# Kernel optimization log

Hardware: AMD Instinct MI355X
Metric: run time of the kernel (lower is better)

The kernel has to match this reference:

```python
import jax, jax.numpy as jnp
import numpy as np

EMBED = 1024
HEADS = 16

def setup_inputs() -> dict:
    key = jax.random.key(0)
    ks = jax.random.split(key, 6)
    N, S = 1, 4096
    half = EMBED // 2
    x = jax.random.normal(ks[0], (N, S, EMBED), dtype=jnp.float32)
    Wq = jax.random.normal(ks[1], (half, half), dtype=jnp.float32) * 0.02
    Wk = jax.random.normal(ks[2], (half, half), dtype=jnp.float32) * 0.02
    Wv = jax.random.normal(ks[3], (half, half), dtype=jnp.float32) * 0.02
    Wo = jax.random.normal(ks[4], (EMBED, half), dtype=jnp.float32) * 0.02
    bo = jnp.zeros((EMBED,), dtype=jnp.float32)
    return {"x": x, "Wq": Wq, "Wk": Wk, "Wv": Wv, "Wo": Wo, "bo": bo}

def reference(x, Wq, Wk, Wv, Wo, bo):
    N, S, E = x.shape
    H = HEADS
    Dh = (E // 2) // H                 # per-head dim of the half-width projections (32)
    scale = float(E // H) ** 0.5       # original scales by head_dim = embed/heads = 64
    left = x[..., : E // 2]            # only the left chunk feeds attention in the source
    # torch Linear: y = x @ W.T (no bias)
    q = (left @ Wq.T).reshape(N, S, H, Dh)
    k = (left @ Wk.T).reshape(N, S, H, Dh)
    v = (left @ Wv.T).reshape(N, S, H, Dh)
    energy = jnp.einsum('nqhd,nkhd->nqkh', q, k)          # [N,S,S,H] full score tensor
    att = jax.nn.softmax(energy / scale, axis=2)          # softmax over key axis
    out = jnp.einsum('nqkh,nkhd->nqhd', att, v)           # [N,S,H,Dh]
    out = out.reshape(N, S, E // 2)
    return out @ Wo.T + bo                                # fc_out: half -> embed
```

## Files before the change

### kernel.cpp

```cpp
#include <hip/hip_runtime.h>
#include <stdint.h>


#define SEQ    4096
#define DMODEL 1024
#define DHALF  512
#define NH     16
#define DH     32

typedef __attribute__((ext_vector_type(4))) float facc4;
typedef __attribute__((ext_vector_type(8))) short bfrag8;

#define MFMA_BF16(a, b, c) __builtin_amdgcn_mfma_f32_16x16x32_bf16((a), (b), (c), 0, 0, 0)

static __device__ __forceinline__ uint16_t f2b(float x) {
    uint32_t u = __float_as_uint(x);
    return (uint16_t)((u + 0x7FFFu + ((u >> 16) & 1u)) >> 16);
}
static __device__ __forceinline__ float b2f(uint16_t b) {
    return __uint_as_float(((uint32_t)b) << 16);
}

static __device__ __forceinline__ bfrag8 cvt8perm(float4 a, float4 b) {
    uint32_t u0 = __float_as_uint(a.x) + 0x8000u, u1 = __float_as_uint(a.y) + 0x8000u;
    uint32_t u2 = __float_as_uint(a.z) + 0x8000u, u3 = __float_as_uint(a.w) + 0x8000u;
    uint32_t u4 = __float_as_uint(b.x) + 0x8000u, u5 = __float_as_uint(b.y) + 0x8000u;
    uint32_t u6 = __float_as_uint(b.z) + 0x8000u, u7 = __float_as_uint(b.w) + 0x8000u;
    union { uint32_t w[4]; bfrag8 r; } u;
    u.w[0] = __builtin_amdgcn_perm(u1, u0, 0x07060302u);
    u.w[1] = __builtin_amdgcn_perm(u3, u2, 0x07060302u);
    u.w[2] = __builtin_amdgcn_perm(u5, u4, 0x07060302u);
    u.w[3] = __builtin_amdgcn_perm(u7, u6, 0x07060302u);
    return u.r;
}

__global__ __launch_bounds__(256) void convert_w(
    const float* __restrict__ Wq, const float* __restrict__ Wk,
    const float* __restrict__ Wv, const float* __restrict__ Wo,
    const float* __restrict__ x,
    uint16_t* __restrict__ q, uint16_t* __restrict__ k,
    uint16_t* __restrict__ v, uint16_t* __restrict__ o,
    uint16_t* __restrict__ xb)
{
    int zz = blockIdx.x;
    if (zz >= 640) {
        size_t g = (size_t)(zz - 640) * 2048 + (size_t)threadIdx.x * 8;
        int row = (int)(g >> 9);
        int col = (int)(g & 511);
        const float* src = &x[(size_t)row * DMODEL + col];
        float4 a = *(const float4*)src;
        float4 b = *(const float4*)(src + 4);
        *(bfrag8*)&xb[g] = cvt8perm(a, b);
        return;
    }
    const float* src; uint16_t* dst; size_t off;
    if      (zz < 128) { src = Wq; dst = q; off = (size_t)zz * 2048; }
    else if (zz < 256) { src = Wk; dst = k; off = (size_t)(zz - 128) * 2048; }
    else if (zz < 384) { src = Wv; dst = v; off = (size_t)(zz - 256) * 2048; }
    else               { src = Wo; dst = o; off = (size_t)(zz - 384) * 2048; }
    size_t i = off + (size_t)threadIdx.x * 8;
    float4 a = *(const float4*)&src[i];
    float4 b = *(const float4*)&src[i + 4];
    *(bfrag8*)&dst[i] = cvt8perm(a, b);
}

__device__ __forceinline__ void gemm128(
    const uint16_t* __restrict__ A, int lda,
    const uint16_t* __restrict__ B, int ldb,
    void* __restrict__ C, int ldc, int cF32,
    const float* __restrict__ bias, float scale,
    int Kd, int m0, int n0)
{
    __shared__ __align__(16) uint16_t As[2][128 * 40];
    __shared__ __align__(16) uint16_t Bs[2][128 * 40];

    const int tid  = threadIdx.x;
    const int lane = tid & 63;
    const int wv   = tid >> 6;
    const int lo   = lane & 15;
    const int quad = lane >> 4;
    const int srow = tid >> 2;
    const int skq  = (tid & 3) * 8;
    const int rb   = (wv >> 1) * 64;
    const int cb   = (wv & 1) * 64;

    const facc4 ZACC = {0.f, 0.f, 0.f, 0.f};
    facc4 acc[4][4];
#pragma unroll
    for (int i = 0; i < 4; ++i)
#pragma unroll
        for (int j = 0; j < 4; ++j) acc[i][j] = ZACC;

    const uint16_t* hA0 = &A[(size_t)(m0 + srow) * lda + skq];
    const uint16_t* hA1 = &A[(size_t)(m0 + srow + 64) * lda + skq];
    const uint16_t* pB0 = &B[(size_t)(n0 + srow) * ldb + skq];
    const uint16_t* pB1 = &B[(size_t)(n0 + srow + 64) * ldb + skq];

    bfrag8 ra0 = *(const bfrag8*)hA0;
    bfrag8 ra1 = *(const bfrag8*)hA1;
    bfrag8 rb0 = *(const bfrag8*)pB0;
    bfrag8 rb1 = *(const bfrag8*)pB1;

    *(bfrag8*)&As[0][srow * 40 + skq]        = ra0;
    *(bfrag8*)&As[0][(srow + 64) * 40 + skq] = ra1;
    *(bfrag8*)&Bs[0][srow * 40 + skq]        = rb0;
    *(bfrag8*)&Bs[0][(srow + 64) * 40 + skq] = rb1;
    __syncthreads();

    int p = 0;
    for (int kt = 0; kt < Kd; kt += 32) {
        const bool more = (kt + 32 < Kd);
        if (more) {
            ra0 = *(const bfrag8*)(hA0 + kt + 32);
            ra1 = *(const bfrag8*)(hA1 + kt + 32);
            rb0 = *(const bfrag8*)(pB0 + kt + 32);
            rb1 = *(const bfrag8*)(pB1 + kt + 32);
        }

        bfrag8 af[4], bf[4];
#pragma unroll
        for (int i = 0; i < 4; ++i) {
            af[i] = *(const bfrag8*)&As[p][(rb + i * 16 + lo) * 40 + quad * 8];
            bf[i] = *(const bfrag8*)&Bs[p][(cb + i * 16 + lo) * 40 + quad * 8];
        }
#pragma unroll
        for (int i = 0; i < 4; ++i)
#pragma unroll
            for (int j = 0; j < 4; ++j)
                acc[i][j] = MFMA_BF16(af[i], bf[j], acc[i][j]);

        if (more) {
            *(bfrag8*)&As[1 - p][srow * 40 + skq]        = ra0;
            *(bfrag8*)&As[1 - p][(srow + 64) * 40 + skq] = ra1;
            *(bfrag8*)&Bs[1 - p][srow * 40 + skq]        = rb0;
            *(bfrag8*)&Bs[1 - p][(srow + 64) * 40 + skq] = rb1;
            __syncthreads();
            p ^= 1;
        }
    }

#pragma unroll
    for (int j = 0; j < 4; ++j) {
        int col  = n0 + cb + j * 16 + lo;
        float bv = bias ? bias[col] : 0.f;
#pragma unroll
        for (int i = 0; i < 4; ++i) {
#pragma unroll
            for (int r = 0; r < 4; ++r) {
                int row = m0 + rb + i * 16 + quad * 4 + r;
                float v = acc[i][j][r] * scale + bv;
                if (cF32) ((float*)C)[(size_t)row * ldc + col] = v;
                else      ((uint16_t*)C)[(size_t)row * ldc + col] = f2b(v);
            }
        }
    }
}

#define SC_Q (0.125f * 1.4426950408889634f)

__global__ __launch_bounds__(256, 2) void qkv_kernel(
    const uint16_t* __restrict__ xb,
    const uint16_t* __restrict__ Wqb, const uint16_t* __restrict__ Wkb,
    const uint16_t* __restrict__ Wvb,
    uint16_t* __restrict__ Q, uint16_t* __restrict__ K, uint16_t* __restrict__ V)
{
    const int z = blockIdx.z;
    const uint16_t* W = (z == 0) ? Wqb : (z == 1) ? Wkb : Wvb;
    uint16_t* Out     = (z == 0) ? Q   : (z == 1) ? K   : V;
    float scale       = (z == 0) ? SC_Q : 1.0f;
    gemm128(xb, DHALF, W, DHALF, Out, DHALF, 0, nullptr, scale, DHALF,
            blockIdx.y * 128, blockIdx.x * 128);
}

__global__ __launch_bounds__(256, 2) void outproj_kernel(
    const uint16_t* __restrict__ O, const uint16_t* __restrict__ Wob,
    const float* __restrict__ bo, float* __restrict__ Y)
{
    gemm128(O, DHALF, Wob, DHALF, Y, DMODEL, 1, bo, 1.0f, DHALF,
            blockIdx.y * 128, blockIdx.x * 128);
}

__global__ __launch_bounds__(256) void attn_kernel(
    const uint16_t* __restrict__ Q, const uint16_t* __restrict__ Kb,
    const uint16_t* __restrict__ Vb, uint16_t* __restrict__ Op,
    float* __restrict__ lbuf, int kspan)
{
    __shared__ __align__(16) uint16_t Ks[2][64 * 40];
    __shared__ __align__(16) uint16_t Vt[2][32 * 64];

    const int tid  = threadIdx.x;
    const int lane = tid & 63;
    const int wv   = tid >> 6;
    const int lo   = lane & 15;
    const int quad = lane >> 4;

    const int f  = blockIdx.x + 32 * blockIdx.y + 512 * blockIdx.z;
    const int pp = (f & 7) | ((f >> 8) << 3);
    const int h  = pp & 15;
    const int sp = pp >> 4;
    const int q0 = ((f >> 3) & 31) * 128;

    const int srow = tid >> 2;
    const int skq  = (tid & 3) * 8;

    const facc4 ZACC = {0.f, 0.f, 0.f, 0.f};

    bfrag8 qf[2];
    qf[0] = *(const bfrag8*)&Q[(size_t)(q0 + wv * 32 + lo) * DHALF + h * DH + quad * 8];
    qf[1] = *(const bfrag8*)&Q[(size_t)(q0 + wv * 32 + 16 + lo) * DHALF + h * DH + quad * 8];

    bfrag8 ones;
#pragma unroll
    for (int j = 0; j < 8; ++j) ones[j] = (short)0x3F80;

    int vt_w[8];
    {
        int pb = ((srow >> 5) << 2) | ((srow >> 2) & 3);
        int pw = (((srow >> 4) & 1) << 2) | (srow & 3);
#pragma unroll
        for (int j = 0; j < 8; ++j) {
            int d  = skq + j;
            int Rd = ((d & 7) + 2 * (d >> 3)) & 7;
            vt_w[j] = d * 64 + (((pb + Rd) & 7) << 3) + pw;
        }
    }
    int vt_r[2][2];
#pragma unroll
    for (int dt = 0; dt < 2; ++dt) {
        int d  = dt * 16 + lo;
        int Rd = ((d & 7) + 2 * (d >> 3)) & 7;
#pragma unroll
        for (int c = 0; c < 2; ++c)
            vt_r[c][dt] = d * 64 + ((((c * 4 + quad) + Rd) & 7) << 3);
    }
    const int ks_r = lo * 40 + quad * 8;

    const uint16_t* kp = &Kb[(size_t)(sp * kspan + srow) * DHALF + h * DH + skq];
    const uint16_t* vp = &Vb[(size_t)(sp * kspan + srow) * DHALF + h * DH + skq];

    facc4 oacc[2][2], oaccL[2];
    oacc[0][0] = ZACC; oacc[0][1] = ZACC;
    oacc[1][0] = ZACC; oacc[1][1] = ZACC;
    oaccL[0] = ZACC; oaccL[1] = ZACC;

    float4 kreg = *(const float4*)kp;
    float4 vreg = *(const float4*)vp;
    kp += 64 * DHALF;
    vp += 64 * DHALF;

#define STAGE(BUF) do {                                                       \
        *(float4*)&Ks[BUF][srow * 40 + skq] = kreg;                           \
        const uint16_t* vsp = (const uint16_t*)&vreg;                         \
        _Pragma("unroll")                                                     \
        for (int j = 0; j < 8; ++j) Vt[BUF][vt_w[j]] = vsp[j];                \
    } while (0)

#define TILE(BUF) do {                                                        \
        uint2 w0[4], w1[4];                                                   \
        _Pragma("unroll")                                                     \
        for (int t4 = 0; t4 < 4; ++t4) {                                      \
            bfrag8 kf = *(const bfrag8*)&Ks[BUF][t4 * 640 + ks_r];            \
            facc4 s0 = MFMA_BF16(kf, qf[0], ZACC);                            \
            facc4 s1 = MFMA_BF16(kf, qf[1], ZACC);                            \
            uint32_t a0 = __float_as_uint(__builtin_amdgcn_exp2f(s0[0])) + 0x8000u; \
            uint32_t a1 = __float_as_uint(__builtin_amdgcn_exp2f(s0[1])) + 0x8000u; \
            uint32_t a2 = __float_as_uint(__builtin_amdgcn_exp2f(s0[2])) + 0x8000u; \
            uint32_t a3 = __float_as_uint(__builtin_amdgcn_exp2f(s0[3])) + 0x8000u; \
            w0[t4].x = __builtin_amdgcn_perm(a1, a0, 0x07060302u);            \
            w0[t4].y = __builtin_amdgcn_perm(a3, a2, 0x07060302u);            \
            uint32_t b0 = __float_as_uint(__builtin_amdgcn_exp2f(s1[0])) + 0x8000u; \
            uint32_t b1 = __float_as_uint(__builtin_amdgcn_exp2f(s1[1])) + 0x8000u; \
            uint32_t b2 = __float_as_uint(__builtin_amdgcn_exp2f(s1[2])) + 0x8000u; \
            uint32_t b3 = __float_as_uint(__builtin_amdgcn_exp2f(s1[3])) + 0x8000u; \
            w1[t4].x = __builtin_amdgcn_perm(b1, b0, 0x07060302u);            \
            w1[t4].y = __builtin_amdgcn_perm(b3, b2, 0x07060302u);            \
        }                                                                     \
        union PU { uint2 u2[2]; bfrag8 f; } pu;                               \
        bfrag8 pf0[2], pf1[2];                                                \
        pu.u2[0] = w0[0]; pu.u2[1] = w0[1]; pf0[0] = pu.f;                    \
        pu.u2[0] = w0[2]; pu.u2[1] = w0[3]; pf0[1] = pu.f;                    \
        pu.u2[0] = w1[0]; pu.u2[1] = w1[1]; pf1[0] = pu.f;                    \
        pu.u2[0] = w1[2]; pu.u2[1] = w1[3]; pf1[1] = pu.f;                    \
        _Pragma("unroll")                                                     \
        for (int c = 0; c < 2; ++c) {                                         \
            _Pragma("unroll")                                                 \
            for (int dt = 0; dt < 2; ++dt) {                                  \
                bfrag8 vf = *(const bfrag8*)&Vt[BUF][vt_r[c][dt]];            \
                oacc[0][dt] = MFMA_BF16(pf0[c], vf, oacc[0][dt]);             \
                oacc[1][dt] = MFMA_BF16(pf1[c], vf, oacc[1][dt]);             \
            }                                                                 \
            oaccL[0] = MFMA_BF16(pf0[c], ones, oaccL[0]);                     \
            oaccL[1] = MFMA_BF16(pf1[c], ones, oaccL[1]);                     \
        }                                                                     \
    } while (0)

    STAGE(0);
    __syncthreads();

    const int nt = kspan >> 6;
    for (int t = 0; t < nt; t += 2) {
        kreg = *(const float4*)kp;
        vreg = *(const float4*)vp;
        kp += 64 * DHALF; vp += 64 * DHALF;
        TILE(0);
        STAGE(1);
        __syncthreads();

        const bool more = (t + 2 < nt);
        if (more) {
            kreg = *(const float4*)kp;
            vreg = *(const float4*)vp;
            kp += 64 * DHALF; vp += 64 * DHALF;
        }
        TILE(1);
        if (more) {
            STAGE(0);
            __syncthreads();
        }
    }
#undef STAGE
#undef TILE

    if (lo == 0) {
#pragma unroll
        for (int g = 0; g < 2; ++g)
#pragma unroll
            for (int r = 0; r < 4; ++r)
                lbuf[((size_t)sp * NH + h) * SEQ + q0 + wv * 32 + g * 16 + quad * 4 + r] =
                    oaccL[g][r];
    }

    uint16_t* Od = Op + (size_t)sp * SEQ * DHALF;
#pragma unroll
    for (int g = 0; g < 2; ++g) {
#pragma unroll
        for (int r = 0; r < 4; ++r) {
            int row = q0 + wv * 32 + g * 16 + quad * 4 + r;
            Od[(size_t)row * DHALF + h * DH + lo]      = f2b(oacc[g][0][r]);
            Od[(size_t)row * DHALF + h * DH + 16 + lo] = f2b(oacc[g][1][r]);
        }
    }
}

__global__ __launch_bounds__(256) void combine_kernel(
    const uint16_t* __restrict__ Op, const float* __restrict__ lbuf,
    uint16_t* __restrict__ O, int ns)
{
    int t   = blockIdx.x * 256 + threadIdx.x;
    int row = t >> 6;
    int cb  = (t & 63) << 3;
    int h   = cb >> 5;
    float l = 0.f;
    float acc[8] = {0.f, 0.f, 0.f, 0.f, 0.f, 0.f, 0.f, 0.f};
    for (int sp = 0; sp < ns; ++sp) {
        l += lbuf[((size_t)sp * NH + h) * SEQ + row];
        bfrag8 a = *(const bfrag8*)&Op[(size_t)sp * SEQ * DHALF + (size_t)row * DHALF + cb];
#pragma unroll
        for (int j = 0; j < 8; ++j) acc[j] += b2f((uint16_t)a[j]);
    }
    float inv = 1.0f / l;
    bfrag8 o;
#pragma unroll
    for (int j = 0; j < 8; ++j) o[j] = (short)f2b(acc[j] * inv);
    *(bfrag8*)&O[(size_t)row * DHALF + cb] = o;
}

extern "C" void kernel_launch(void* const* d_in, const int* in_sizes, int n_in,
                              void* d_out, int out_size, void* d_ws, size_t ws_size,
                              hipStream_t stream)
{
    const float* x  = (const float*)d_in[0];
    const float* Wq = (const float*)d_in[1];
    const float* Wk = (const float*)d_in[2];
    const float* Wv = (const float*)d_in[3];
    const float* Wo = (const float*)d_in[4];
    const float* bo = (const float*)d_in[5];

    size_t fixed_e = 3 * (size_t)DHALF * DHALF + (size_t)DMODEL * DHALF
                   + 4 * (size_t)SEQ * DHALF;
    size_t need4 = (fixed_e + 4 * (size_t)SEQ * DHALF) * 2
                 + 4 * (size_t)NH * SEQ * 4;
    const int ns = (ws_size >= need4) ? 4 : 2;

    uint16_t* Wqb = (uint16_t*)d_ws;
    uint16_t* Wkb = Wqb + (size_t)DHALF * DHALF;
    uint16_t* Wvb = Wkb + (size_t)DHALF * DHALF;
    uint16_t* Wob = Wvb + (size_t)DHALF * DHALF;
    uint16_t* Q   = Wob + (size_t)DMODEL * DHALF;
    uint16_t* K   = Q + (size_t)SEQ * DHALF;
    uint16_t* V   = K + (size_t)SEQ * DHALF;
    uint16_t* O   = V + (size_t)SEQ * DHALF;
    uint16_t* Op  = O + (size_t)SEQ * DHALF;
    float*  lbuf  = (float*)(Op + (size_t)ns * SEQ * DHALF);
    uint16_t* xb  = O;

    convert_w<<<1664, 256, 0, stream>>>(Wq, Wk, Wv, Wo, x, Wqb, Wkb, Wvb, Wob, xb);
    qkv_kernel<<<dim3(DHALF / 128, SEQ / 128, 3), 256, 0, stream>>>(
        xb, Wqb, Wkb, Wvb, Q, K, V);
    attn_kernel<<<dim3(SEQ / 128, NH, ns), 256, 0, stream>>>(Q, K, V, Op, lbuf, SEQ / ns);
    combine_kernel<<<1024, 256, 0, stream>>>(Op, lbuf, O, ns);
    outproj_kernel<<<dim3(DMODEL / 128, SEQ / 128), 256, 0, stream>>>(
        O, Wob, bo, (float*)d_out);
}
```

Measured before the change: 169.2 us.

## Use 64x128 GEMM tiles with transposed MFMA output for vectorized stores

Halves the M tile of the shared projection GEMM so the QKV and output projection launch twice as many blocks, improving CU fill on a wide GPU. Swaps MFMA operand order so each lane holds four consecutive output columns, enabling float4/packed bf16 stores and a vector bias load instead of scalar writes. The trade-off is lower per-block data reuse and more redundant loads of the B operand.

Result: no change. 172.0 us (+1.7%).

```diff
diff --git a/kernel.cpp b/kernel.cpp
--- a/kernel.cpp
+++ b/kernel.cpp
@@ -64,14 +64,14 @@
     *(bfrag8*)&dst[i] = cvt8perm(a, b);
 }
 
-__device__ __forceinline__ void gemm128(
+__device__ __forceinline__ void gemm64x128(
     const uint16_t* __restrict__ A, int lda,
     const uint16_t* __restrict__ B, int ldb,
     void* __restrict__ C, int ldc, int cF32,
     const float* __restrict__ bias, float scale,
     int Kd, int m0, int n0)
 {
-    __shared__ __align__(16) uint16_t As[2][128 * 40];
+    __shared__ __align__(16) uint16_t As[2][64 * 40];
     __shared__ __align__(16) uint16_t Bs[2][128 * 40];
 
     const int tid  = threadIdx.x;
@@ -81,28 +81,25 @@
     const int quad = lane >> 4;
     const int srow = tid >> 2;
     const int skq  = (tid & 3) * 8;
-    const int rb   = (wv >> 1) * 64;
-    const int cb   = (wv & 1) * 64;
+    const int rt   = (wv >> 1) * 32;
+    const int ct   = (wv & 1) * 64;
 
     const facc4 ZACC = {0.f, 0.f, 0.f, 0.f};
-    facc4 acc[4][4];
-#pragma unroll
-    for (int i = 0; i < 4; ++i)
+    facc4 acc[2][4];
+#pragma unroll
+    for (int i = 0; i < 2; ++i)
 #pragma unroll
         for (int j = 0; j < 4; ++j) acc[i][j] = ZACC;
 
-    const uint16_t* hA0 = &A[(size_t)(m0 + srow) * lda + skq];
-    const uint16_t* hA1 = &A[(size_t)(m0 + srow + 64) * lda + skq];
+    const uint16_t* hA  = &A[(size_t)(m0 + srow) * lda + skq];
     const uint16_t* pB0 = &B[(size_t)(n0 + srow) * ldb + skq];
     const uint16_t* pB1 = &B[(size_t)(n0 + srow + 64) * ldb + skq];
 
-    bfrag8 ra0 = *(const bfrag8*)hA0;
-    bfrag8 ra1 = *(const bfrag8*)hA1;
+    bfrag8 ra  = *(const bfrag8*)hA;
     bfrag8 rb0 = *(const bfrag8*)pB0;
     bfrag8 rb1 = *(const bfrag8*)pB1;
 
-    *(bfrag8*)&As[0][srow * 40 + skq]        = ra0;
-    *(bfrag8*)&As[0][(srow + 64) * 40 + skq] = ra1;
+    *(bfrag8*)&As[0][srow * 40 + skq]        = ra;
     *(bfrag8*)&Bs[0][srow * 40 + skq]        = rb0;
     *(bfrag8*)&Bs[0][(srow + 64) * 40 + skq] = rb1;
     __syncthreads();
@@ -111,27 +108,26 @@
     for (int kt = 0; kt < Kd; kt += 32) {
         const bool more = (kt + 32 < Kd);
         if (more) {
-            ra0 = *(const bfrag8*)(hA0 + kt + 32);
-            ra1 = *(const bfrag8*)(hA1 + kt + 32);
+            ra  = *(const bfrag8*)(hA + kt + 32);
             rb0 = *(const bfrag8*)(pB0 + kt + 32);
             rb1 = *(const bfrag8*)(pB1 + kt + 32);
         }
 
-        bfrag8 af[4], bf[4];
-#pragma unroll
-        for (int i = 0; i < 4; ++i) {
-            af[i] = *(const bfrag8*)&As[p][(rb + i * 16 + lo) * 40 + quad * 8];
-            bf[i] = *(const bfrag8*)&Bs[p][(cb + i * 16 + lo) * 40 + quad * 8];
-        }
-#pragma unroll
-        for (int i = 0; i < 4; ++i)
+        bfrag8 af[2], bf[4];
+#pragma unroll
+        for (int i = 0; i < 2; ++i)
+            af[i] = *(const bfrag8*)&As[p][(rt + i * 16 + lo) * 40 + quad * 8];
+#pragma unroll
+        for (int j = 0; j < 4; ++j)
+            bf[j] = *(const bfrag8*)&Bs[p][(ct + j * 16 + lo) * 40 + quad * 8];
+#pragma unroll
+        for (int i = 0; i < 2; ++i)
 #pragma unroll
             for (int j = 0; j < 4; ++j)
-                acc[i][j] = MFMA_BF16(af[i], bf[j], acc[i][j]);
+                acc[i][j] = MFMA_BF16(bf[j], af[i], acc[i][j]);
 
         if (more) {
-            *(bfrag8*)&As[1 - p][srow * 40 + skq]        = ra0;
-            *(bfrag8*)&As[1 - p][(srow + 64) * 40 + skq] = ra1;
+            *(bfrag8*)&As[1 - p][srow * 40 + skq]        = ra;
             *(bfrag8*)&Bs[1 - p][srow * 40 + skq]        = rb0;
             *(bfrag8*)&Bs[1 - p][(srow + 64) * 40 + skq] = rb1;
             __syncthreads();
@@ -140,17 +136,25 @@
     }
 
 #pragma unroll
-    for (int j = 0; j < 4; ++j) {
-        int col  = n0 + cb + j * 16 + lo;
-        float bv = bias ? bias[col] : 0.f;
-#pragma unroll
-        for (int i = 0; i < 4; ++i) {
-#pragma unroll
-            for (int r = 0; r < 4; ++r) {
-                int row = m0 + rb + i * 16 + quad * 4 + r;
-                float v = acc[i][j][r] * scale + bv;
-                if (cF32) ((float*)C)[(size_t)row * ldc + col] = v;
-                else      ((uint16_t*)C)[(size_t)row * ldc + col] = f2b(v);
+    for (int i = 0; i < 2; ++i) {
+        const size_t row = (size_t)(m0 + rt + i * 16 + lo);
+#pragma unroll
+        for (int j = 0; j < 4; ++j) {
+            const int colb = n0 + ct + j * 16 + quad * 4;
+            float4 bv = {0.f, 0.f, 0.f, 0.f};
+            if (bias) bv = *(const float4*)&bias[colb];
+            float v0 = acc[i][j][0] * scale + bv.x;
+            float v1 = acc[i][j][1] * scale + bv.y;
+            float v2 = acc[i][j][2] * scale + bv.z;
+            float v3 = acc[i][j][3] * scale + bv.w;
+            if (cF32) {
+                float4 o = {v0, v1, v2, v3};
+                *(float4*)&((float*)C)[row * ldc + colb] = o;
+            } else {
+                uint2 o;
+                o.x = (uint32_t)f2b(v0) | ((uint32_t)f2b(v1) << 16);
+                o.y = (uint32_t)f2b(v2) | ((uint32_t)f2b(v3) << 16);
+                *(uint2*)&((uint16_t*)C)[row * ldc + colb] = o;
             }
         }
     }
@@ -168,16 +172,16 @@
     const uint16_t* W = (z == 0) ? Wqb : (z == 1) ? Wkb : Wvb;
     uint16_t* Out     = (z == 0) ? Q   : (z == 1) ? K   : V;
     float scale       = (z == 0) ? SC_Q : 1.0f;
-    gemm128(xb, DHALF, W, DHALF, Out, DHALF, 0, nullptr, scale, DHALF,
-            blockIdx.y * 128, blockIdx.x * 128);
+    gemm64x128(xb, DHALF, W, DHALF, Out, DHALF, 0, nullptr, scale, DHALF,
+               blockIdx.y * 64, blockIdx.x * 128);
 }
 
 __global__ __launch_bounds__(256, 2) void outproj_kernel(
     const uint16_t* __restrict__ O, const uint16_t* __restrict__ Wob,
     const float* __restrict__ bo, float* __restrict__ Y)
 {
-    gemm128(O, DHALF, Wob, DHALF, Y, DMODEL, 1, bo, 1.0f, DHALF,
-            blockIdx.y * 128, blockIdx.x * 128);
+    gemm64x128(O, DHALF, Wob, DHALF, Y, DMODEL, 1, bo, 1.0f, DHALF,
+               blockIdx.y * 64, blockIdx.x * 128);
 }
 
 __global__ __launch_bounds__(256) void attn_kernel(
@@ -395,10 +399,10 @@
     uint16_t* xb  = O;
 
     convert_w<<<1664, 256, 0, stream>>>(Wq, Wk, Wv, Wo, x, Wqb, Wkb, Wvb, Wob, xb);
-    qkv_kernel<<<dim3(DHALF / 128, SEQ / 128, 3), 256, 0, stream>>>(
+    qkv_kernel<<<dim3(DHALF / 128, SEQ / 64, 3), 256, 0, stream>>>(
         xb, Wqb, Wkb, Wvb, Q, K, V);
     attn_kernel<<<dim3(SEQ / 128, NH, ns), 256, 0, stream>>>(Q, K, V, Op, lbuf, SEQ / ns);
     combine_kernel<<<1024, 256, 0, stream>>>(Op, lbuf, O, ns);
-    outproj_kernel<<<dim3(DMODEL / 128, SEQ / 128), 256, 0, stream>>>(
+    outproj_kernel<<<dim3(DMODEL / 128, SEQ / 64), 256, 0, stream>>>(
         O, Wob, bo, (float*)d_out);
 }
```

## Enlarge attention blocks to 512 threads with 128-key tiles; vectorize GEMM epilogue

Applied to the files above, without the earlier changes.

The attention kernel now runs 512-thread blocks covering 256 queries and stages 128-key K/V tiles per step. This halves the number of barrier-separated iterations and shares each staged tile across more waves. The GEMM swaps the MFMA operand order so each lane holds contiguous output columns, which lets the epilogue use vectorized float4/uint2 stores and a float4 bias load instead of scalar stores. Larger blocks and doubled LDS use per block may lower occupancy and reduce the number of blocks available to fill the GPU.

Result: faster. 163.5 us (-3.3%).

```diff
diff --git a/kernel.cpp b/kernel.cpp
--- a/kernel.cpp
+++ b/kernel.cpp
@@ -127,7 +127,7 @@
         for (int i = 0; i < 4; ++i)
 #pragma unroll
             for (int j = 0; j < 4; ++j)
-                acc[i][j] = MFMA_BF16(af[i], bf[j], acc[i][j]);
+                acc[i][j] = MFMA_BF16(bf[j], af[i], acc[i][j]);
 
         if (more) {
             *(bfrag8*)&As[1 - p][srow * 40 + skq]        = ra0;
@@ -140,17 +140,25 @@
     }
 
 #pragma unroll
-    for (int j = 0; j < 4; ++j) {
-        int col  = n0 + cb + j * 16 + lo;
-        float bv = bias ? bias[col] : 0.f;
-#pragma unroll
-        for (int i = 0; i < 4; ++i) {
-#pragma unroll
-            for (int r = 0; r < 4; ++r) {
-                int row = m0 + rb + i * 16 + quad * 4 + r;
-                float v = acc[i][j][r] * scale + bv;
-                if (cF32) ((float*)C)[(size_t)row * ldc + col] = v;
-                else      ((uint16_t*)C)[(size_t)row * ldc + col] = f2b(v);
+    for (int i = 0; i < 4; ++i) {
+        const size_t row = (size_t)(m0 + rb + i * 16 + lo);
+#pragma unroll
+        for (int j = 0; j < 4; ++j) {
+            const int colb = n0 + cb + j * 16 + quad * 4;
+            float4 bv = {0.f, 0.f, 0.f, 0.f};
+            if (bias) bv = *(const float4*)&bias[colb];
+            float v0 = acc[i][j][0] * scale + bv.x;
+            float v1 = acc[i][j][1] * scale + bv.y;
+            float v2 = acc[i][j][2] * scale + bv.z;
+            float v3 = acc[i][j][3] * scale + bv.w;
+            if (cF32) {
+                float4 o = {v0, v1, v2, v3};
+                *(float4*)&((float*)C)[row * ldc + colb] = o;
+            } else {
+                uint2 o;
+                o.x = (uint32_t)f2b(v0) | ((uint32_t)f2b(v1) << 16);
+                o.y = (uint32_t)f2b(v2) | ((uint32_t)f2b(v3) << 16);
+                *(uint2*)&((uint16_t*)C)[row * ldc + colb] = o;
             }
         }
     }
@@ -180,13 +188,13 @@
             blockIdx.y * 128, blockIdx.x * 128);
 }
 
-__global__ __launch_bounds__(256) void attn_kernel(
+__global__ __launch_bounds__(512) void attn_kernel(
     const uint16_t* __restrict__ Q, const uint16_t* __restrict__ Kb,
     const uint16_t* __restrict__ Vb, uint16_t* __restrict__ Op,
     float* __restrict__ lbuf, int kspan)
 {
-    __shared__ __align__(16) uint16_t Ks[2][64 * 40];
-    __shared__ __align__(16) uint16_t Vt[2][32 * 64];
+    __shared__ __align__(16) uint16_t Ks[2][128 * 40];
+    __shared__ __align__(16) uint16_t Vt[2][32 * 128];
 
     const int tid  = threadIdx.x;
     const int lane = tid & 63;
@@ -194,11 +202,11 @@
     const int lo   = lane & 15;
     const int quad = lane >> 4;
 
-    const int f  = blockIdx.x + 32 * blockIdx.y + 512 * blockIdx.z;
-    const int pp = (f & 7) | ((f >> 8) << 3);
+    const int f  = blockIdx.x + 16 * blockIdx.y + 256 * blockIdx.z;
+    const int pp = (f & 7) | ((f >> 7) << 3);
     const int h  = pp & 15;
     const int sp = pp >> 4;
-    const int q0 = ((f >> 3) & 31) * 128;
+    const int q0 = ((f >> 3) & 15) * 256;
 
     const int srow = tid >> 2;
     const int skq  = (tid & 3) * 8;
@@ -221,17 +229,17 @@
         for (int j = 0; j < 8; ++j) {
             int d  = skq + j;
             int Rd = ((d & 7) + 2 * (d >> 3)) & 7;
-            vt_w[j] = d * 64 + (((pb + Rd) & 7) << 3) + pw;
-        }
-    }
-    int vt_r[2][2];
+            vt_w[j] = d * 128 + (((pb + Rd) & 15) << 3) + pw;
+        }
+    }
+    int vt_r[4][2];
 #pragma unroll
     for (int dt = 0; dt < 2; ++dt) {
         int d  = dt * 16 + lo;
         int Rd = ((d & 7) + 2 * (d >> 3)) & 7;
 #pragma unroll
-        for (int c = 0; c < 2; ++c)
-            vt_r[c][dt] = d * 64 + ((((c * 4 + quad) + Rd) & 7) << 3);
+        for (int c = 0; c < 4; ++c)
+            vt_r[c][dt] = d * 128 + ((((c * 4 + quad) + Rd) & 15) << 3);
     }
     const int ks_r = lo * 40 + quad * 8;
 
@@ -245,8 +253,8 @@
 
     float4 kreg = *(const float4*)kp;
     float4 vreg = *(const float4*)vp;
-    kp += 64 * DHALF;
-    vp += 64 * DHALF;
+    kp += 128 * DHALF;
+    vp += 128 * DHALF;
 
 #define STAGE(BUF) do {                                                       \
         *(float4*)&Ks[BUF][srow * 40 + skq] = kreg;                           \
@@ -255,11 +263,11 @@
         for (int j = 0; j < 8; ++j) Vt[BUF][vt_w[j]] = vsp[j];                \
     } while (0)
 
-#define TILE(BUF) do {                                                        \
+#define HALF(BUF, HH) do {                                                    \
         uint2 w0[4], w1[4];                                                   \
         _Pragma("unroll")                                                     \
         for (int t4 = 0; t4 < 4; ++t4) {                                      \
-            bfrag8 kf = *(const bfrag8*)&Ks[BUF][t4 * 640 + ks_r];            \
+            bfrag8 kf = *(const bfrag8*)&Ks[BUF][(4 * HH + t4) * 640 + ks_r]; \
             facc4 s0 = MFMA_BF16(kf, qf[0], ZACC);                            \
             facc4 s1 = MFMA_BF16(kf, qf[1], ZACC);                            \
             uint32_t a0 = __float_as_uint(__builtin_amdgcn_exp2f(s0[0])) + 0x8000u; \
@@ -282,26 +290,28 @@
         pu.u2[0] = w1[0]; pu.u2[1] = w1[1]; pf1[0] = pu.f;                    \
         pu.u2[0] = w1[2]; pu.u2[1] = w1[3]; pf1[1] = pu.f;                    \
         _Pragma("unroll")                                                     \
-        for (int c = 0; c < 2; ++c) {                                         \
+        for (int cc = 0; cc < 2; ++cc) {                                      \
             _Pragma("unroll")                                                 \
             for (int dt = 0; dt < 2; ++dt) {                                  \
-                bfrag8 vf = *(const bfrag8*)&Vt[BUF][vt_r[c][dt]];            \
-                oacc[0][dt] = MFMA_BF16(pf0[c], vf, oacc[0][dt]);             \
-                oacc[1][dt] = MFMA_BF16(pf1[c], vf, oacc[1][dt]);             \
+                bfrag8 vf = *(const bfrag8*)&Vt[BUF][vt_r[2 * HH + cc][dt]];  \
+                oacc[0][dt] = MFMA_BF16(pf0[cc], vf, oacc[0][dt]);            \
+                oacc[1][dt] = MFMA_BF16(pf1[cc], vf, oacc[1][dt]);            \
             }                                                                 \
-            oaccL[0] = MFMA_BF16(pf0[c], ones, oaccL[0]);                     \
-            oaccL[1] = MFMA_BF16(pf1[c], ones, oaccL[1]);                     \
+            oaccL[0] = MFMA_BF16(pf0[cc], ones, oaccL[0]);                    \
+            oaccL[1] = MFMA_BF16(pf1[cc], ones, oaccL[1]);                    \
         }                                                                     \
     } while (0)
 
+#define TILE(BUF) do { HALF(BUF, 0); HALF(BUF, 1); } while (0)
+
     STAGE(0);
     __syncthreads();
 
-    const int nt = kspan >> 6;
+    const int nt = kspan >> 7;
     for (int t = 0; t < nt; t += 2) {
         kreg = *(const float4*)kp;
         vreg = *(const float4*)vp;
-        kp += 64 * DHALF; vp += 64 * DHALF;
+        kp += 128 * DHALF; vp += 128 * DHALF;
         TILE(0);
         STAGE(1);
         __syncthreads();
@@ -310,7 +320,7 @@
         if (more) {
             kreg = *(const float4*)kp;
             vreg = *(const float4*)vp;
-            kp += 64 * DHALF; vp += 64 * DHALF;
+            kp += 128 * DHALF; vp += 128 * DHALF;
         }
         TILE(1);
         if (more) {
@@ -319,6 +329,7 @@
         }
     }
 #undef STAGE
+#undef HALF
 #undef TILE
 
     if (lo == 0) {
@@ -397,7 +408,7 @@
     convert_w<<<1664, 256, 0, stream>>>(Wq, Wk, Wv, Wo, x, Wqb, Wkb, Wvb, Wob, xb);
     qkv_kernel<<<dim3(DHALF / 128, SEQ / 128, 3), 256, 0, stream>>>(
         xb, Wqb, Wkb, Wvb, Q, K, V);
-    attn_kernel<<<dim3(SEQ / 128, NH, ns), 256, 0, stream>>>(Q, K, V, Op, lbuf, SEQ / ns);
+    attn_kernel<<<dim3(SEQ / 256, NH, ns), 512, 0, stream>>>(Q, K, V, Op, lbuf, SEQ / ns);
     combine_kernel<<<1024, 256, 0, stream>>>(Op, lbuf, O, ns);
     outproj_kernel<<<dim3(DMODEL / 128, SEQ / 128), 256, 0, stream>>>(
         O, Wob, bo, (float*)d_out);
```
